# Optimization experiments

Measured on AMD Instinct MI355X. Metric: run time of the kernel, lower is better.

Reference implementation:

```python
import jax, jax.numpy as jnp
import numpy as np

EPS = 1e-6

def elu_feature_map(x):
    return jax.nn.elu(x) + 1.0

def setup_inputs() -> dict:
    key = jax.random.key(0)
    k1, k2, k3 = jax.random.split(key, 3)
    N, S, H, D, M = 16, 4096, 16, 64, 64
    query = jax.random.normal(k1, (N, H, D), dtype=jnp.float32)
    keys = jax.random.normal(k2, (N, S, H, D), dtype=jnp.float32)
    values = jax.random.normal(k3, (N, S, H, M), dtype=jnp.float32)
    key_mask = jnp.ones((N, S), dtype=jnp.float32)  # key_lengths.float_matrix
    return {"query": query, "keys": keys, "values": values, "key_mask": key_mask}

def reference(query, keys, values, key_mask):
    # Q: [N,H,D]
    Q = elu_feature_map(query)
    # K: [N,S,H,D], masked over sequence
    K = elu_feature_map(keys) * key_mask[:, :, None, None]
    # S_state: [N,H,M,D] -- K^T V outer-product reduction over sequence
    S_state = jnp.einsum('nshd,nshm->nhmd', K, values)
    # Z: [N,H,D] -- normalizer
    Z = K.sum(axis=1)
    # QZ: [N,H]
    QZ = 1.0 / (jnp.einsum('nhd,nhd->nh', Q, Z) + EPS)
    # V_out: [N,H,M]
    V_out = jnp.einsum('nhd,nhmd,nh->nhm', Q, S_state, QZ)
    return (V_out, S_state, Z)
```

## Files before the change

kernel.cpp:

```cpp
#include <hip/hip_runtime.h>


#define S_LEN  4096
#define NHEAD  16
#define DDIM   64
#define MDIM   64
#define NWAVE  8
#define RPW    (S_LEN / NWAVE)
#define CH_S   32
#define NCHK   (RPW / CH_S)
#define KP32   20

#define OUT_SOFF  (16 * 16 * 64)
#define OUT_ZOFF  (OUT_SOFF + 16 * 16 * 64 * 64)

using short8 = __attribute__((ext_vector_type(8))) short;
using f32x4  = __attribute__((ext_vector_type(4))) float;
using uint4v = __attribute__((ext_vector_type(4))) unsigned int;

union FragCast { uint4v u; short8 s; };

__device__ __forceinline__ float elup1(float x) {
    return x > 0.0f ? x + 1.0f : __expf(x);
}

__device__ __forceinline__ unsigned bfpack(float a, float b) {
    union { float f; unsigned u; } ca, cb;
    ca.f = a; cb.f = b;
    const unsigned ra = ca.u + 0x7FFFu + ((ca.u >> 16) & 1u);
    const unsigned rb = cb.u + 0x7FFFu + ((cb.u >> 16) & 1u);
    return (ra >> 16) | (rb & 0xFFFF0000u);
}

__global__ __launch_bounds__(512, 1)
void rcla_mfma(const float* __restrict__ query,
               const float* __restrict__ keys,
               const float* __restrict__ values,
               const float* __restrict__ kmask,
               float* __restrict__ out)
{
    __shared__ unsigned Ktu[NWAVE][DDIM][KP32];
    __shared__ unsigned Vtu[NWAVE][MDIM][KP32];
    __shared__ float buf2[2][64][68];
    __shared__ float zb2[2][DDIM];
    __shared__ float qb[DDIM];

    const int t    = threadIdx.x;
    const int wave = t >> 6;
    const int lane = t & 63;
    const int c16  = lane & 15;
    const int g    = lane >> 4;
    const int pair = blockIdx.x;
    const int nIdx = pair >> 4;
    const int hIdx = pair & 15;

    const int d0s  = c16 * 4;

    const size_t rowStride = (size_t)NHEAD * DDIM;
    const size_t base = ((size_t)nIdx * S_LEN + (size_t)wave * RPW) * rowStride
                      + (size_t)hIdx * DDIM;
    const float* kbase = keys   + base;
    const float* vbase = values + base;
    const float* mbase = kmask + (size_t)nIdx * S_LEN + wave * RPW;

    f32x4 acc[4][4];
#pragma unroll
    for (int i = 0; i < 4; ++i)
#pragma unroll
        for (int j = 0; j < 4; ++j) acc[i][j] = f32x4{0.f, 0.f, 0.f, 0.f};
    float4 zacc = make_float4(0.f, 0.f, 0.f, 0.f);

    for (int ch = 0; ch < NCHK; ++ch) {
        const int scg = ch * CH_S + g * 8;

#pragma unroll
        for (int q = 0; q < 4; ++q) {
            const int sp = g * 4 + q;
            const int sl = scg + 2 * q;
            const float* kp = kbase + (size_t)sl * rowStride + d0s;
            const float4 k1 = *(const float4*)kp;
            const float4 k2 = *(const float4*)(kp + rowStride);
            const float2 mm = *(const float2*)(mbase + sl);
            const float a0 = elup1(k1.x) * mm.x, a1 = elup1(k1.y) * mm.x;
            const float a2 = elup1(k1.z) * mm.x, a3 = elup1(k1.w) * mm.x;
            const float b0 = elup1(k2.x) * mm.y, b1 = elup1(k2.y) * mm.y;
            const float b2 = elup1(k2.z) * mm.y, b3 = elup1(k2.w) * mm.y;
            zacc.x += a0 + b0;  zacc.y += a1 + b1;
            zacc.z += a2 + b2;  zacc.w += a3 + b3;
            Ktu[wave][d0s + 0][sp] = bfpack(a0, b0);
            Ktu[wave][d0s + 1][sp] = bfpack(a1, b1);
            Ktu[wave][d0s + 2][sp] = bfpack(a2, b2);
            Ktu[wave][d0s + 3][sp] = bfpack(a3, b3);
        }

#pragma unroll
        for (int q = 0; q < 4; ++q) {
            const int sp = g * 4 + q;
            const int sl = scg + 2 * q;
            const float* vp = vbase + (size_t)sl * rowStride + d0s;
            const float4 v1 = *(const float4*)vp;
            const float4 v2 = *(const float4*)(vp + rowStride);
            Vtu[wave][d0s + 0][sp] = bfpack(v1.x, v2.x);
            Vtu[wave][d0s + 1][sp] = bfpack(v1.y, v2.y);
            Vtu[wave][d0s + 2][sp] = bfpack(v1.z, v2.z);
            Vtu[wave][d0s + 3][sp] = bfpack(v1.w, v2.w);
        }

        asm volatile("" ::: "memory");

        short8 af[4], bff[4];
#pragma unroll
        for (int ti = 0; ti < 4; ++ti) {
            FragCast fc;
            fc.u = *(const uint4v*)&Vtu[wave][ti * 16 + c16][g * 4];
            af[ti] = fc.s;
        }
#pragma unroll
        for (int tj = 0; tj < 4; ++tj) {
            FragCast fc;
            fc.u = *(const uint4v*)&Ktu[wave][tj * 16 + c16][g * 4];
            bff[tj] = fc.s;
        }

        asm volatile("" ::: "memory");

#pragma unroll
        for (int ti = 0; ti < 4; ++ti)
#pragma unroll
            for (int tj = 0; tj < 4; ++tj)
                acc[ti][tj] = __builtin_amdgcn_mfma_f32_16x16x32_bf16(
                    af[ti], bff[tj], acc[ti][tj], 0, 0, 0);
    }

    zacc.x += __shfl_xor(zacc.x, 16, 64); zacc.y += __shfl_xor(zacc.y, 16, 64);
    zacc.z += __shfl_xor(zacc.z, 16, 64); zacc.w += __shfl_xor(zacc.w, 16, 64);
    zacc.x += __shfl_xor(zacc.x, 32, 64); zacc.y += __shfl_xor(zacc.y, 32, 64);
    zacc.z += __shfl_xor(zacc.z, 32, 64); zacc.w += __shfl_xor(zacc.w, 32, 64);

    __syncthreads();
    if (t < DDIM) qb[t] = elup1(query[(size_t)pair * DDIM + t]);

    const int grp = wave >> 2;
    for (int rr = 0; rr < 4; ++rr) {
        if ((wave & 3) == rr) {
#pragma unroll
            for (int ti = 0; ti < 4; ++ti)
#pragma unroll
                for (int tj = 0; tj < 4; ++tj)
#pragma unroll
                    for (int r = 0; r < 4; ++r) {
                        const int m = ti * 16 + g * 4 + r;
                        const int d = tj * 16 + c16;
                        if (rr == 0) buf2[grp][m][d]  = acc[ti][tj][r];
                        else         buf2[grp][m][d] += acc[ti][tj][r];
                    }
            if (lane < 16) {
                if (rr == 0) {
                    zb2[grp][d0s]     = zacc.x;  zb2[grp][d0s + 1] = zacc.y;
                    zb2[grp][d0s + 2] = zacc.z;  zb2[grp][d0s + 3] = zacc.w;
                } else {
                    zb2[grp][d0s]     += zacc.x; zb2[grp][d0s + 1] += zacc.y;
                    zb2[grp][d0s + 2] += zacc.z; zb2[grp][d0s + 3] += zacc.w;
                }
            }
        }
        __syncthreads();
    }

    {
        const int m  = t >> 3;
        const int dc = (t & 7) * 8;
        float4 a0 = *(const float4*)&buf2[0][m][dc];
        float4 a1 = *(const float4*)&buf2[0][m][dc + 4];
        const float4 b0 = *(const float4*)&buf2[1][m][dc];
        const float4 b1 = *(const float4*)&buf2[1][m][dc + 4];
        a0.x += b0.x; a0.y += b0.y; a0.z += b0.z; a0.w += b0.w;
        a1.x += b1.x; a1.y += b1.y; a1.z += b1.z; a1.w += b1.w;
        float* dst = out + OUT_SOFF + ((size_t)pair * MDIM + m) * DDIM + dc;
        *(float4*)dst       = a0;
        *(float4*)(dst + 4) = a1;
        *(float4*)&buf2[0][m][dc]     = a0;
        *(float4*)&buf2[0][m][dc + 4] = a1;
    }
    if (t < DDIM) {
        const float zv = zb2[0][t] + zb2[1][t];
        out[OUT_ZOFF + (size_t)pair * DDIM + t] = zv;
        zb2[0][t] = zv;
    }
    __syncthreads();

    if (wave == 0) {
        float zp = qb[lane] * zb2[0][lane];
#pragma unroll
        for (int off = 32; off >= 1; off >>= 1) zp += __shfl_xor(zp, off, 64);
        const float qz = 1.0f / (zp + 1e-6f);
        float vs = 0.0f;
#pragma unroll
        for (int d = 0; d < DDIM; d += 4) {
            const float4 sv = *(const float4*)&buf2[0][lane][d];
            vs = fmaf(qb[d],     sv.x, vs);
            vs = fmaf(qb[d + 1], sv.y, vs);
            vs = fmaf(qb[d + 2], sv.z, vs);
            vs = fmaf(qb[d + 3], sv.w, vs);
        }
        out[(size_t)pair * MDIM + lane] = qz * vs;
    }
}

extern "C" void kernel_launch(void* const* d_in, const int* in_sizes, int n_in,
                              void* d_out, int out_size, void* d_ws, size_t ws_size,
                              hipStream_t stream) {
    const float* q  = (const float*)d_in[0];
    const float* k  = (const float*)d_in[1];
    const float* v  = (const float*)d_in[2];
    const float* km = (const float*)d_in[3];
    float* out = (float*)d_out;
    rcla_mfma<<<dim3(256), dim3(512), 0, stream>>>(q, k, v, km, out);
}
```

Baseline: 103.5 us.

## Split sequence across blocks with workspace partials and a separate reduce kernel

Replaces the single 256-block kernel, one block per (n,h) pair, with a partial kernel that splits each pair's sequence into up to four parts. Each block runs 4 waves and writes partial S and Z sums to workspace, then a second kernel adds the partials and computes the normalizer and output. The aim is more blocks, and so better occupancy, on a GPU with many CUs. It also packs the LDS transpose writes into 128-bit stores and overlays the staging and reduction LDS buffers in a union. The cost is an extra launch plus workspace write and read traffic, and the split falls back to fewer parts if the workspace is too small.

```diff
diff --git a/kernel.cpp b/kernel.cpp
--- a/kernel.cpp
+++ b/kernel.cpp
@@ -5,11 +5,10 @@
 #define NHEAD  16
 #define DDIM   64
 #define MDIM   64
-#define NWAVE  8
-#define RPW    (S_LEN / NWAVE)
+#define NWAVE  4
 #define CH_S   32
-#define NCHK   (RPW / CH_S)
 #define KP32   20
+#define WS_ROW 4160
 
 #define OUT_SOFF  (16 * 16 * 64)
 #define OUT_ZOFF  (OUT_SOFF + 16 * 16 * 64 * 64)
@@ -32,36 +31,44 @@
     return (ra >> 16) | (rb & 0xFFFF0000u);
 }
 
-__global__ __launch_bounds__(512, 1)
-void rcla_mfma(const float* __restrict__ query,
-               const float* __restrict__ keys,
-               const float* __restrict__ values,
-               const float* __restrict__ kmask,
-               float* __restrict__ out)
+union SmemT {
+    struct {
+        unsigned Kt[NWAVE][DDIM][KP32];
+        unsigned Vt[NWAVE][MDIM][KP32];
+    } h;
+    struct {
+        float buf[2][64][68];
+        float zb[2][64];
+    } m;
+};
+
+__global__ __launch_bounds__(256, 4)
+void rcla_partial(const float* __restrict__ keys,
+                  const float* __restrict__ values,
+                  const float* __restrict__ kmask,
+                  float* __restrict__ ws,
+                  int nchk, int psh)
 {
-    __shared__ unsigned Ktu[NWAVE][DDIM][KP32];
-    __shared__ unsigned Vtu[NWAVE][MDIM][KP32];
-    __shared__ float buf2[2][64][68];
-    __shared__ float zb2[2][DDIM];
-    __shared__ float qb[DDIM];
+    __shared__ SmemT sm;
 
     const int t    = threadIdx.x;
     const int wave = t >> 6;
     const int lane = t & 63;
     const int c16  = lane & 15;
     const int g    = lane >> 4;
-    const int pair = blockIdx.x;
+    const int part = blockIdx.x & ((1 << psh) - 1);
+    const int pair = blockIdx.x >> psh;
     const int nIdx = pair >> 4;
     const int hIdx = pair & 15;
-
     const int d0s  = c16 * 4;
 
     const size_t rowStride = (size_t)NHEAD * DDIM;
-    const size_t base = ((size_t)nIdx * S_LEN + (size_t)wave * RPW) * rowStride
+    const int sWave = part * (S_LEN >> psh) + wave * (nchk * CH_S);
+    const size_t base = ((size_t)nIdx * S_LEN + sWave) * rowStride
                       + (size_t)hIdx * DDIM;
     const float* kbase = keys   + base;
     const float* vbase = values + base;
-    const float* mbase = kmask + (size_t)nIdx * S_LEN + wave * RPW;
+    const float* mbase = kmask + (size_t)nIdx * S_LEN + sWave;
 
     f32x4 acc[4][4];
 #pragma unroll
@@ -70,12 +77,12 @@
         for (int j = 0; j < 4; ++j) acc[i][j] = f32x4{0.f, 0.f, 0.f, 0.f};
     float4 zacc = make_float4(0.f, 0.f, 0.f, 0.f);
 
-    for (int ch = 0; ch < NCHK; ++ch) {
+    for (int ch = 0; ch < nchk; ++ch) {
         const int scg = ch * CH_S + g * 8;
+        unsigned kw[16];
 
 #pragma unroll
         for (int q = 0; q < 4; ++q) {
-            const int sp = g * 4 + q;
             const int sl = scg + 2 * q;
             const float* kp = kbase + (size_t)sl * rowStride + d0s;
             const float4 k1 = *(const float4*)kp;
@@ -87,23 +94,32 @@
             const float b2 = elup1(k2.z) * mm.y, b3 = elup1(k2.w) * mm.y;
             zacc.x += a0 + b0;  zacc.y += a1 + b1;
             zacc.z += a2 + b2;  zacc.w += a3 + b3;
-            Ktu[wave][d0s + 0][sp] = bfpack(a0, b0);
-            Ktu[wave][d0s + 1][sp] = bfpack(a1, b1);
-            Ktu[wave][d0s + 2][sp] = bfpack(a2, b2);
-            Ktu[wave][d0s + 3][sp] = bfpack(a3, b3);
+            kw[0 * 4 + q] = bfpack(a0, b0);
+            kw[1 * 4 + q] = bfpack(a1, b1);
+            kw[2 * 4 + q] = bfpack(a2, b2);
+            kw[3 * 4 + q] = bfpack(a3, b3);
+        }
+#pragma unroll
+        for (int i = 0; i < 4; ++i) {
+            uint4v w = {kw[i * 4 + 0], kw[i * 4 + 1], kw[i * 4 + 2], kw[i * 4 + 3]};
+            *(uint4v*)&sm.h.Kt[wave][d0s + i][g * 4] = w;
         }
 
 #pragma unroll
         for (int q = 0; q < 4; ++q) {
-            const int sp = g * 4 + q;
             const int sl = scg + 2 * q;
             const float* vp = vbase + (size_t)sl * rowStride + d0s;
             const float4 v1 = *(const float4*)vp;
             const float4 v2 = *(const float4*)(vp + rowStride);
-            Vtu[wave][d0s + 0][sp] = bfpack(v1.x, v2.x);
-            Vtu[wave][d0s + 1][sp] = bfpack(v1.y, v2.y);
-            Vtu[wave][d0s + 2][sp] = bfpack(v1.z, v2.z);
-            Vtu[wave][d0s + 3][sp] = bfpack(v1.w, v2.w);
+            kw[0 * 4 + q] = bfpack(v1.x, v2.x);
+            kw[1 * 4 + q] = bfpack(v1.y, v2.y);
+            kw[2 * 4 + q] = bfpack(v1.z, v2.z);
+            kw[3 * 4 + q] = bfpack(v1.w, v2.w);
+        }
+#pragma unroll
+        for (int i = 0; i < 4; ++i) {
+            uint4v w = {kw[i * 4 + 0], kw[i * 4 + 1], kw[i * 4 + 2], kw[i * 4 + 3]};
+            *(uint4v*)&sm.h.Vt[wave][d0s + i][g * 4] = w;
         }
 
         asm volatile("" ::: "memory");
@@ -112,13 +128,13 @@
 #pragma unroll
         for (int ti = 0; ti < 4; ++ti) {
             FragCast fc;
-            fc.u = *(const uint4v*)&Vtu[wave][ti * 16 + c16][g * 4];
+            fc.u = *(const uint4v*)&sm.h.Vt[wave][ti * 16 + c16][g * 4];
             af[ti] = fc.s;
         }
 #pragma unroll
         for (int tj = 0; tj < 4; ++tj) {
             FragCast fc;
-            fc.u = *(const uint4v*)&Ktu[wave][tj * 16 + c16][g * 4];
+            fc.u = *(const uint4v*)&sm.h.Kt[wave][tj * 16 + c16][g * 4];
             bff[tj] = fc.s;
         }
 
@@ -138,11 +154,10 @@
     zacc.z += __shfl_xor(zacc.z, 32, 64); zacc.w += __shfl_xor(zacc.w, 32, 64);
 
     __syncthreads();
-    if (t < DDIM) qb[t] = elup1(query[(size_t)pair * DDIM + t]);
-
-    const int grp = wave >> 2;
-    for (int rr = 0; rr < 4; ++rr) {
-        if ((wave & 3) == rr) {
+
+    const int grp = wave >> 1;
+    for (int rr = 0; rr < 2; ++rr) {
+        if ((wave & 1) == rr) {
 #pragma unroll
             for (int ti = 0; ti < 4; ++ti)
 #pragma unroll
@@ -151,59 +166,94 @@
                     for (int r = 0; r < 4; ++r) {
                         const int m = ti * 16 + g * 4 + r;
                         const int d = tj * 16 + c16;
-                        if (rr == 0) buf2[grp][m][d]  = acc[ti][tj][r];
-                        else         buf2[grp][m][d] += acc[ti][tj][r];
+                        if (rr == 0) sm.m.buf[grp][m][d]  = acc[ti][tj][r];
+                        else         sm.m.buf[grp][m][d] += acc[ti][tj][r];
                     }
             if (lane < 16) {
                 if (rr == 0) {
-                    zb2[grp][d0s]     = zacc.x;  zb2[grp][d0s + 1] = zacc.y;
-                    zb2[grp][d0s + 2] = zacc.z;  zb2[grp][d0s + 3] = zacc.w;
+                    sm.m.zb[grp][d0s]     = zacc.x;  sm.m.zb[grp][d0s + 1] = zacc.y;
+                    sm.m.zb[grp][d0s + 2] = zacc.z;  sm.m.zb[grp][d0s + 3] = zacc.w;
                 } else {
-                    zb2[grp][d0s]     += zacc.x; zb2[grp][d0s + 1] += zacc.y;
-                    zb2[grp][d0s + 2] += zacc.z; zb2[grp][d0s + 3] += zacc.w;
+                    sm.m.zb[grp][d0s]     += zacc.x; sm.m.zb[grp][d0s + 1] += zacc.y;
+                    sm.m.zb[grp][d0s + 2] += zacc.z; sm.m.zb[grp][d0s + 3] += zacc.w;
                 }
             }
         }
         __syncthreads();
     }
 
+    float* wrow = ws + (size_t)blockIdx.x * WS_ROW;
     {
-        const int m  = t >> 3;
-        const int dc = (t & 7) * 8;
-        float4 a0 = *(const float4*)&buf2[0][m][dc];
-        float4 a1 = *(const float4*)&buf2[0][m][dc + 4];
-        const float4 b0 = *(const float4*)&buf2[1][m][dc];
-        const float4 b1 = *(const float4*)&buf2[1][m][dc + 4];
-        a0.x += b0.x; a0.y += b0.y; a0.z += b0.z; a0.w += b0.w;
-        a1.x += b1.x; a1.y += b1.y; a1.z += b1.z; a1.w += b1.w;
-        float* dst = out + OUT_SOFF + ((size_t)pair * MDIM + m) * DDIM + dc;
-        *(float4*)dst       = a0;
-        *(float4*)(dst + 4) = a1;
-        *(float4*)&buf2[0][m][dc]     = a0;
-        *(float4*)&buf2[0][m][dc + 4] = a1;
-    }
-    if (t < DDIM) {
-        const float zv = zb2[0][t] + zb2[1][t];
-        out[OUT_ZOFF + (size_t)pair * DDIM + t] = zv;
-        zb2[0][t] = zv;
+        const int m  = t >> 2;
+        const int dc = (t & 3) * 16;
+#pragma unroll
+        for (int j = 0; j < 16; j += 4) {
+            float4 a = *(const float4*)&sm.m.buf[0][m][dc + j];
+            const float4 b = *(const float4*)&sm.m.buf[1][m][dc + j];
+            a.x += b.x; a.y += b.y; a.z += b.z; a.w += b.w;
+            *(float4*)&wrow[m * 64 + dc + j] = a;
+        }
+    }
+    if (t < DDIM) wrow[64 * 64 + t] = sm.m.zb[0][t] + sm.m.zb[1][t];
+}
+
+__global__ __launch_bounds__(256)
+void rcla_reduce(const float* __restrict__ query,
+                 const float* __restrict__ ws,
+                 float* __restrict__ out,
+                 int nsplit)
+{
+    __shared__ float S[64][68];
+    __shared__ float zb[64];
+    __shared__ float qb[64];
+
+    const int p = blockIdx.x;
+    const int t = threadIdx.x;
+    const float* bp = ws + (size_t)p * nsplit * WS_ROW;
+
+    const int m  = t >> 2;
+    const int dc = (t & 3) * 16;
+    float4 a[4];
+#pragma unroll
+    for (int j = 0; j < 4; ++j) a[j] = make_float4(0.f, 0.f, 0.f, 0.f);
+    for (int part = 0; part < nsplit; ++part) {
+        const float* w = bp + (size_t)part * WS_ROW + m * 64 + dc;
+#pragma unroll
+        for (int j = 0; j < 4; ++j) {
+            const float4 x = *(const float4*)&w[j * 4];
+            a[j].x += x.x; a[j].y += x.y; a[j].z += x.z; a[j].w += x.w;
+        }
+    }
+#pragma unroll
+    for (int j = 0; j < 4; ++j) {
+        *(float4*)&out[OUT_SOFF + (size_t)p * 4096 + m * 64 + dc + j * 4] = a[j];
+        *(float4*)&S[m][dc + j * 4] = a[j];
+    }
+    if (t < 64) {
+        float zv = 0.f;
+        for (int part = 0; part < nsplit; ++part)
+            zv += bp[(size_t)part * WS_ROW + 64 * 64 + t];
+        out[OUT_ZOFF + (size_t)p * 64 + t] = zv;
+        zb[t] = zv;
+        qb[t] = elup1(query[(size_t)p * 64 + t]);
     }
     __syncthreads();
 
-    if (wave == 0) {
-        float zp = qb[lane] * zb2[0][lane];
+    if (t < 64) {
+        float zp = qb[t] * zb[t];
 #pragma unroll
         for (int off = 32; off >= 1; off >>= 1) zp += __shfl_xor(zp, off, 64);
         const float qz = 1.0f / (zp + 1e-6f);
         float vs = 0.0f;
 #pragma unroll
-        for (int d = 0; d < DDIM; d += 4) {
-            const float4 sv = *(const float4*)&buf2[0][lane][d];
+        for (int d = 0; d < 64; d += 4) {
+            const float4 sv = *(const float4*)&S[t][d];
             vs = fmaf(qb[d],     sv.x, vs);
             vs = fmaf(qb[d + 1], sv.y, vs);
             vs = fmaf(qb[d + 2], sv.z, vs);
             vs = fmaf(qb[d + 3], sv.w, vs);
         }
-        out[(size_t)pair * MDIM + lane] = qz * vs;
+        out[(size_t)p * 64 + t] = qz * vs;
     }
 }
 
@@ -215,5 +265,14 @@
     const float* v  = (const float*)d_in[2];
     const float* km = (const float*)d_in[3];
     float* out = (float*)d_out;
-    rcla_mfma<<<dim3(256), dim3(512), 0, stream>>>(q, k, v, km, out);
-}
+    float* wsf = (float*)d_ws;
+
+    int psh = 2;
+    if (ws_size < (size_t)256 * 4 * WS_ROW * sizeof(float)) psh = 1;
+    if (ws_size < (size_t)256 * 2 * WS_ROW * sizeof(float)) psh = 0;
+    const int split = 1 << psh;
+    const int nchk  = (S_LEN >> psh) / (NWAVE * CH_S);
+
+    rcla_partial<<<dim3(256 * split), dim3(256), 0, stream>>>(k, v, km, wsf, nchk, psh);
+    rcla_reduce <<<dim3(256),         dim3(256), 0, stream>>>(q, wsf, out, split);
+}
```

New measurement: 180.8 us. 1.75x slower.
